# Kernel tuning notes

Hardware: AMD Instinct MI355X
Metric: run time of the kernel (lower is better)

Reference implementation:

```python
import jax, jax.numpy as jnp
import numpy as np

GS = 7        # grid_size
NB = 2        # num_boxes
NC = 20       # num_classes
THR = 0.5     # NMS threshold (source default)
IMG = 448.0   # max_size used in _encode_outputs


def _nms_keep(boxes, scores, valid, thr):
    """Faithful port of the source's (inverted) greedy NMS.

    Picks the highest-score alive box, keeps it, then RETAINS only boxes
    with IoU >= thr against it (discarding low-overlap ones), repeating.
    Fixed-shape: returns a bool keep-mask of length N.
    """
    N = scores.shape[0]
    x1, y1, x2, y2 = boxes[:, 0], boxes[:, 1], boxes[:, 2], boxes[:, 3]
    areas = (x2 - x1) * (y2 - y1)
    neg = jnp.asarray(-1e30, scores.dtype)
    idx = jnp.arange(N)

    def step(carry, _):
        alive, keep = carry
        any_alive = jnp.any(alive)
        i = jnp.argmax(jnp.where(alive, scores, neg))
        keep = keep | ((idx == i) & any_alive)
        ix1 = jnp.maximum(x1, x1[i]); iy1 = jnp.maximum(y1, y1[i])
        ix2 = jnp.minimum(x2, x2[i]); iy2 = jnp.minimum(y2, y2[i])
        inter = jnp.clip(ix2 - ix1, 0) * jnp.clip(iy2 - iy1, 0)
        iou = inter / (areas[i] + areas - inter)
        new_alive = (alive & (iou >= thr)) & (idx != i)
        alive = jnp.where(any_alive, new_alive, alive)
        return (alive, keep), None

    (_, keep), _ = jax.lax.scan(step, (valid, jnp.zeros(N, bool)), None, length=N)
    return keep


def _forward(x, W, b):
    B = x.shape[0]
    out = (x @ W.T + b).reshape(B, GS, GS, 5 * NB + NC)  # (B,7,7,30)
    cell = 1.0 / GS
    g = jnp.arange(GS, dtype=out.dtype) * cell
    norm_x = g[None, None, :]   # varies along last grid axis (grid_x[r,c]=c)
    norm_y = g[None, :, None]

    labels = out[..., 5 * NB:]                                # (B,7,7,20)
    labels_proba = jnp.argmax(labels, -1).astype(out.dtype)   # class index

    N = B * GS * GS
    labels_flat = labels.reshape(N, NC)

    slot_boxes, slot_scores, slot_valid = [], [], []
    for off in range(0, 5 * NB, 5):
        bx = out[..., off:off + 4]
        sc = out[..., off + 5]                 # faithful off-by-one in source
        valid = (sc * labels_proba) > 0.5      # faithful score*class_index mask
        cx = bx[..., 0] * cell + norm_x
        cy = bx[..., 1] * cell + norm_y
        w_, h_ = bx[..., 2], bx[..., 3]
        X1 = cx - 0.5 * w_; Y1 = cy - 0.5 * h_
        X2 = cx + 0.5 * w_; Y2 = cy + 0.5 * h_
        # NMS applies xywh2xyxy AGAIN on already-xyxy boxes (faithful):
        bb = jnp.stack([X1 - X2 / 2, Y1 - Y2 / 2, X1 + X2 / 2, Y1 + Y2 / 2], -1)
        slot_boxes.append(bb.reshape(N, 4))
        slot_scores.append(sc.reshape(N))
        slot_valid.append(valid.reshape(N))

    boxes = jnp.stack(slot_boxes)     # (NB, N, 4)
    scores = jnp.stack(slot_scores)   # (NB, N)
    valid = jnp.stack(slot_valid)     # (NB, N)

    keep = jax.vmap(_nms_keep, in_axes=(0, 0, 0, None))(boxes, scores, valid, THR)

    labels_all = jnp.broadcast_to(labels_flat[None], (NB, N, NC))
    packed = jnp.concatenate([boxes * IMG, scores[..., None], labels_all], -1)
    return packed * keep[..., None].astype(packed.dtype)  # (NB, N, 25)


def setup_inputs() -> dict:
    key = jax.random.key(0)
    k1, k2, k3 = jax.random.split(key, 3)
    B = 64
    x = jax.random.normal(k1, (B, 2304), jnp.float32)
    W = jax.random.normal(k2, (1470, 2304), jnp.float32) * 0.02
    b = jax.random.normal(k3, (1470,), jnp.float32) * 0.01
    return {"x": x, "W": W, "b": b}


def reference(x, W, b):
    return _forward(x, W, b)
```

## Files before the change

### kernel.cpp

```cpp
#include <hip/hip_runtime.h>

#define B_     64
#define KDIM   2304
#define NCOL   1470
#define NCELL  3136
#define CPAD   1536
#define SPLITK 16
#define KCHUNK 144
#define NSTAGE 9
#define XS     68
#define WSD    100
#define NMS_T  1024
#define QMAX   4

__global__ __launch_bounds__(256) void gemm_splitk(
    const float* __restrict__ x, const float* __restrict__ W,
    float* __restrict__ partial)
{
    __shared__ float sx[2][16 * XS];
    __shared__ float sw[2][16 * WSD];

    const int t   = threadIdx.x;
    const int c0  = blockIdx.x * 96;
    const int k0  = blockIdx.y * KCHUNK;
    const int r8  = (t >> 5) << 3;
    const int cgi = t & 31;
    const int kk0 = t & 15;
    const int g0  = t >> 4;

    float acc[8][3];
#pragma unroll
    for (int i = 0; i < 8; ++i)
#pragma unroll
        for (int j = 0; j < 3; ++j) acc[i][j] = 0.f;

    const float* wp[6];
#pragma unroll
    for (int p = 0; p < 6; ++p) {
        int gc = c0 + p * 16 + g0;
        if (gc >= NCOL) gc = NCOL - 1;
        wp[p] = W + (size_t)gc * KDIM + kk0;
    }

    float xr[4], wr[6];
    {
        const int kb = k0;
#pragma unroll
        for (int p = 0; p < 4; ++p) xr[p] = x[(p * 16 + g0) * KDIM + kb + kk0];
#pragma unroll
        for (int p = 0; p < 6; ++p) wr[p] = wp[p][kb];
#pragma unroll
        for (int p = 0; p < 4; ++p) sx[0][kk0 * XS + p * 16 + g0] = xr[p];
#pragma unroll
        for (int p = 0; p < 6; ++p) sw[0][kk0 * WSD + p * 16 + g0] = wr[p];
    }

    for (int s = 0; s < NSTAGE; ++s) {
        const int cb = s & 1;
        if (s + 1 < NSTAGE) {
            const int kb = k0 + ((s + 1) << 4);
#pragma unroll
            for (int p = 0; p < 4; ++p) xr[p] = x[(p * 16 + g0) * KDIM + kb + kk0];
#pragma unroll
            for (int p = 0; p < 6; ++p) wr[p] = wp[p][kb];
        }
        __syncthreads();
        const float* cx = sx[cb];
        const float* cw = sw[cb];
#pragma unroll
        for (int kk = 0; kk < 16; ++kk) {
            const float4 a0 = *(const float4*)&cx[kk * XS + r8];
            const float4 a1 = *(const float4*)&cx[kk * XS + r8 + 4];
            const float w0 = cw[kk * WSD + cgi];
            const float w1 = cw[kk * WSD + cgi + 32];
            const float w2 = cw[kk * WSD + cgi + 64];
            const float av[8] = {a0.x, a0.y, a0.z, a0.w, a1.x, a1.y, a1.z, a1.w};
#pragma unroll
            for (int i = 0; i < 8; ++i) {
                acc[i][0] = fmaf(av[i], w0, acc[i][0]);
                acc[i][1] = fmaf(av[i], w1, acc[i][1]);
                acc[i][2] = fmaf(av[i], w2, acc[i][2]);
            }
        }
        if (s + 1 < NSTAGE) {
#pragma unroll
            for (int p = 0; p < 4; ++p) sx[cb ^ 1][kk0 * XS + p * 16 + g0] = xr[p];
#pragma unroll
            for (int p = 0; p < 6; ++p) sw[cb ^ 1][kk0 * WSD + p * 16 + g0] = wr[p];
        }
    }

    float* pb = partial + (size_t)blockIdx.y * (B_ * CPAD) + c0 + cgi;
#pragma unroll
    for (int i = 0; i < 8; ++i)
#pragma unroll
        for (int p = 0; p < 3; ++p)
            pb[(size_t)(r8 + i) * CPAD + 32 * p] = acc[i][p];
}

__global__ __launch_bounds__(256) void combine_prep(
    const float* __restrict__ partial, const float* __restrict__ bias,
    float* __restrict__ labels, float* __restrict__ boxes,
    float* __restrict__ scores, int* __restrict__ valid)
{
    __shared__ float sa[8][30];
    const int t    = threadIdx.x;
    const int base = blockIdx.x * 8;

    if (t < 240) {
        const int n   = base + t / 30;
        const int col = t % 30;
        const int row = n / 49;
        const int cr  = (n % 49) * 30 + col;
        float s = 0.f;
#pragma unroll
        for (int k = 0; k < SPLITK; ++k)
            s += partial[(size_t)k * (B_ * CPAD) + (size_t)row * CPAD + cr];
        s += bias[cr];
        sa[t / 30][col] = s;
        if (col >= 10) labels[(size_t)n * 20 + (col - 10)] = s;
    }
    __syncthreads();

    if (t < 8) {
        const int n = base + t;
        const float* a = sa[t];
        float mv = a[10]; int mi = 0;
#pragma unroll
        for (int j = 1; j < 20; ++j) {
            float v = a[10 + j];
            if (v > mv) { mv = v; mi = j; }
        }
        const float lp = (float)mi;
        const int gx = n % 7, gy = (n / 7) % 7;
        const float cw = 1.0f / 7.0f;
        const float nx = (float)gx * cw, ny = (float)gy * cw;
#pragma unroll
        for (int sl = 0; sl < 2; ++sl) {
            const int off = 5 * sl;
            const float bx0 = a[off], bx1 = a[off + 1];
            const float w_ = a[off + 2], h_ = a[off + 3];
            const float sc = a[off + 5];
            const float cx = bx0 * cw + nx, cy = bx1 * cw + ny;
            const float X1 = cx - 0.5f * w_, Y1 = cy - 0.5f * h_;
            const float X2 = cx + 0.5f * w_, Y2 = cy + 0.5f * h_;
            const int m = sl * NCELL + n;
            boxes[m * 4 + 0] = X1 - 0.5f * X2;
            boxes[m * 4 + 1] = Y1 - 0.5f * Y2;
            boxes[m * 4 + 2] = X1 + 0.5f * X2;
            boxes[m * 4 + 3] = Y1 + 0.5f * Y2;
            scores[m] = sc;
            valid[m] = (sc * lp > 0.5f) ? 1 : 0;
        }
    }
}

__global__ __launch_bounds__(NMS_T) void nms_kernel(
    const float* __restrict__ boxes, const float* __restrict__ scores,
    const int* __restrict__ valid, float* __restrict__ keep)
{
    __shared__ float sX1[NCELL], sY1[NCELL], sX2[NCELL], sY2[NCELL];
    __shared__ float sSc[NCELL];
    __shared__ unsigned char kp[NCELL];
    __shared__ float rv[16];
    __shared__ int   rn[16];
    __shared__ int   pickN;

    const int slot = blockIdx.x;
    const int base = slot * NCELL;
    const int t = threadIdx.x;

    unsigned am = 0;
#pragma unroll
    for (int q = 0; q < QMAX; ++q) {
        const int n = t + q * NMS_T;
        if (n < NCELL) {
            const float4 bb = *(const float4*)&boxes[(size_t)(base + n) * 4];
            sX1[n] = bb.x; sY1[n] = bb.y; sX2[n] = bb.z; sY2[n] = bb.w;
            sSc[n] = scores[base + n];
            kp[n] = 0;
            if (valid[base + n]) am |= 1u << q;
        }
    }
    __syncthreads();

    for (;;) {
        float bv = -1e30f; int bn = 0x7fffffff;
#pragma unroll
        for (int q = 0; q < QMAX; ++q)
            if ((am >> q) & 1u) {
                const int n = t + q * NMS_T;
                const float v = sSc[n];
                if (v > bv || (v == bv && n < bn)) { bv = v; bn = n; }
            }
#pragma unroll
        for (int o = 32; o > 0; o >>= 1) {
            const float ov = __shfl_down(bv, o);
            const int   on = __shfl_down(bn, o);
            if (ov > bv || (ov == bv && on < bn)) { bv = ov; bn = on; }
        }
        if ((t & 63) == 0) { rv[t >> 6] = bv; rn[t >> 6] = bn; }
        __syncthreads();
        if (t == 0) {
            float v2 = rv[0]; int n2 = rn[0];
#pragma unroll
            for (int q = 1; q < 16; ++q)
                if (rv[q] > v2 || (rv[q] == v2 && rn[q] < n2)) { v2 = rv[q]; n2 = rn[q]; }
            if (v2 == -1e30f) { pickN = -1; }
            else { pickN = n2; kp[n2] = 1; }
        }
        __syncthreads();
        const int pn = pickN;
        if (pn < 0) break;
        const float px1 = sX1[pn], py1 = sY1[pn], px2 = sX2[pn], py2 = sY2[pn];
        const float pa = (px2 - px1) * (py2 - py1);

#pragma unroll
        for (int q = 0; q < QMAX; ++q)
            if ((am >> q) & 1u) {
                const int n = t + q * NMS_T;
                const float x1 = sX1[n], y1 = sY1[n], x2 = sX2[n], y2 = sY2[n];
                const float an = (x2 - x1) * (y2 - y1);
                const float ix1 = fmaxf(x1, px1), iy1 = fmaxf(y1, py1);
                const float ix2 = fminf(x2, px2), iy2 = fminf(y2, py2);
                const float inter = fmaxf(ix2 - ix1, 0.f) * fmaxf(iy2 - iy1, 0.f);
                const float iou = inter / (pa + an - inter);
                if (!(iou >= 0.5f) || n == pn) am &= ~(1u << q);
            }
    }

    for (int n = t; n < NCELL; n += NMS_T)
        keep[base + n] = (float)kp[n];
}

__global__ void pack_out(const float* __restrict__ labels,
                         const float* __restrict__ boxes,
                         const float* __restrict__ scores,
                         const float* __restrict__ keep,
                         float* __restrict__ out)
{
    int idx = blockIdx.x * 256 + threadIdx.x;
    if (idx >= 2 * NCELL * 25) return;
    int c  = idx % 25;
    int sn = idx / 25;
    int n  = sn % NCELL;
    float k = keep[sn];
    float v;
    if (c < 4)       v = boxes[(size_t)sn * 4 + c] * 448.0f;
    else if (c == 4) v = scores[sn];
    else             v = labels[(size_t)n * 20 + (c - 5)];
    out[idx] = v * k;
}

extern "C" void kernel_launch(void* const* d_in, const int* in_sizes, int n_in,
                              void* d_out, int out_size, void* d_ws, size_t ws_size,
                              hipStream_t stream)
{
    const float* x = (const float*)d_in[0];
    const float* W = (const float*)d_in[1];
    const float* b = (const float*)d_in[2];
    float* out = (float*)d_out;

    float* ws      = (float*)d_ws;
    float* partial = ws;
    float* labels  = partial + (size_t)SPLITK * B_ * CPAD;
    float* boxes   = labels + (size_t)NCELL * 20;
    float* scores  = boxes + (size_t)NCELL * 8;
    int*   valid   = (int*)(scores + (size_t)NCELL * 2);
    float* keep    = (float*)(valid + (size_t)NCELL * 2);

    hipLaunchKernelGGL(gemm_splitk, dim3(16, SPLITK), dim3(256), 0, stream,
                       x, W, partial);
    hipLaunchKernelGGL(combine_prep, dim3(NCELL / 8), dim3(256), 0, stream,
                       partial, b, labels, boxes, scores, valid);
    hipLaunchKernelGGL(nms_kernel, dim3(2), dim3(NMS_T), 0, stream,
                       boxes, scores, valid, keep);
    hipLaunchKernelGGL(pack_out, dim3((2 * NCELL * 25 + 255) / 256), dim3(256), 0, stream,
                       labels, boxes, scores, keep, out);
}
```

Before: 33.04 us.

## Fuse output packing into NMS and zero output inside GEMM kernel

Removes the separate pack_out kernel. The GEMM blocks now zero the whole output buffer up front. The NMS kernel records the list of picked indices and writes only the kept rows of the output, taking box coordinates and scores from shared memory. This saves one kernel launch and the full keep-mask round trip, at the cost of serial pick-list appends and a tail write loop inside the two-block NMS kernel.

```diff
diff --git a/kernel.cpp b/kernel.cpp
--- a/kernel.cpp
+++ b/kernel.cpp
@@ -12,15 +12,23 @@
 #define WSD    100
 #define NMS_T  1024
 #define QMAX   4
+#define OUTSZ  (2 * NCELL * 25)
 
 __global__ __launch_bounds__(256) void gemm_splitk(
     const float* __restrict__ x, const float* __restrict__ W,
-    float* __restrict__ partial)
+    float* __restrict__ partial, float* __restrict__ out)
 {
     __shared__ float sx[2][16 * XS];
     __shared__ float sw[2][16 * WSD];
 
-    const int t   = threadIdx.x;
+    const int t = threadIdx.x;
+
+    {
+        const int gt = (blockIdx.y * 16 + blockIdx.x) * 256 + t;
+        if (gt < OUTSZ / 4)
+            *(float4*)&out[gt * 4] = make_float4(0.f, 0.f, 0.f, 0.f);
+    }
+
     const int c0  = blockIdx.x * 96;
     const int k0  = blockIdx.y * KCHUNK;
     const int r8  = (t >> 5) << 3;
@@ -155,21 +163,23 @@
     }
 }
 
-__global__ __launch_bounds__(NMS_T) void nms_kernel(
+__global__ __launch_bounds__(NMS_T) void nms_pick(
     const float* __restrict__ boxes, const float* __restrict__ scores,
-    const int* __restrict__ valid, float* __restrict__ keep)
+    const int* __restrict__ valid, const float* __restrict__ labels,
+    float* __restrict__ out)
 {
     __shared__ float sX1[NCELL], sY1[NCELL], sX2[NCELL], sY2[NCELL];
     __shared__ float sSc[NCELL];
-    __shared__ unsigned char kp[NCELL];
+    __shared__ int   pickList[NCELL];
     __shared__ float rv[16];
     __shared__ int   rn[16];
-    __shared__ int   pickN;
+    __shared__ int   pickN, npicks;
 
     const int slot = blockIdx.x;
     const int base = slot * NCELL;
     const int t = threadIdx.x;
 
+    if (t == 0) npicks = 0;
     unsigned am = 0;
 #pragma unroll
     for (int q = 0; q < QMAX; ++q) {
@@ -178,7 +188,6 @@
             const float4 bb = *(const float4*)&boxes[(size_t)(base + n) * 4];
             sX1[n] = bb.x; sY1[n] = bb.y; sX2[n] = bb.z; sY2[n] = bb.w;
             sSc[n] = scores[base + n];
-            kp[n] = 0;
             if (valid[base + n]) am |= 1u << q;
         }
     }
@@ -207,7 +216,7 @@
             for (int q = 1; q < 16; ++q)
                 if (rv[q] > v2 || (rv[q] == v2 && rn[q] < n2)) { v2 = rv[q]; n2 = rn[q]; }
             if (v2 == -1e30f) { pickN = -1; }
-            else { pickN = n2; kp[n2] = 1; }
+            else { pickN = n2; pickList[npicks++] = n2; }
         }
         __syncthreads();
         const int pn = pickN;
@@ -229,27 +238,17 @@
             }
     }
 
-    for (int n = t; n < NCELL; n += NMS_T)
-        keep[base + n] = (float)kp[n];
-}
-
-__global__ void pack_out(const float* __restrict__ labels,
-                         const float* __restrict__ boxes,
-                         const float* __restrict__ scores,
-                         const float* __restrict__ keep,
-                         float* __restrict__ out)
-{
-    int idx = blockIdx.x * 256 + threadIdx.x;
-    if (idx >= 2 * NCELL * 25) return;
-    int c  = idx % 25;
-    int sn = idx / 25;
-    int n  = sn % NCELL;
-    float k = keep[sn];
-    float v;
-    if (c < 4)       v = boxes[(size_t)sn * 4 + c] * 448.0f;
-    else if (c == 4) v = scores[sn];
-    else             v = labels[(size_t)n * 20 + (c - 5)];
-    out[idx] = v * k;
+    const int np = npicks;
+    for (int u = t; u < np * 25; u += NMS_T) {
+        const int pi = u / 25;
+        const int c  = u % 25;
+        const int n  = pickList[pi];
+        float v;
+        if (c < 4)       v = (c == 0 ? sX1[n] : c == 1 ? sY1[n] : c == 2 ? sX2[n] : sY2[n]) * 448.0f;
+        else if (c == 4) v = sSc[n];
+        else             v = labels[(size_t)n * 20 + (c - 5)];
+        out[(size_t)(base + n) * 25 + c] = v;
+    }
 }
 
 extern "C" void kernel_launch(void* const* d_in, const int* in_sizes, int n_in,
@@ -267,14 +266,11 @@
     float* boxes   = labels + (size_t)NCELL * 20;
     float* scores  = boxes + (size_t)NCELL * 8;
     int*   valid   = (int*)(scores + (size_t)NCELL * 2);
-    float* keep    = (float*)(valid + (size_t)NCELL * 2);
 
     hipLaunchKernelGGL(gemm_splitk, dim3(16, SPLITK), dim3(256), 0, stream,
-                       x, W, partial);
+                       x, W, partial, out);
     hipLaunchKernelGGL(combine_prep, dim3(NCELL / 8), dim3(256), 0, stream,
                        partial, b, labels, boxes, scores, valid);
-    hipLaunchKernelGGL(nms_kernel, dim3(2), dim3(NMS_T), 0, stream,
-                       boxes, scores, valid, keep);
-    hipLaunchKernelGGL(pack_out, dim3((2 * NCELL * 25 + 255) / 256), dim3(256), 0, stream,
-                       labels, boxes, scores, keep, out);
-}
+    hipLaunchKernelGGL(nms_pick, dim3(2), dim3(NMS_T), 0, stream,
+                       boxes, scores, valid, labels, out);
+}
```

After: 30.95 us (median of 2 runs). 1.07x faster.
